# Optimization experiments

Hardware: AMD Instinct MI355X
Metric: run time of the kernel (lower is better)

Reference implementation:

```python
import jax, jax.numpy as jnp
import numpy as np

B_, C_, H_, W_ = 8, 512, 64, 64

def conv1x1(x, W, b):
    # 1x1 conv == per-pixel linear: [B,C,H,W] x [O,C] -> [B,O,H,W]
    return jnp.einsum('bchw,oc->bohw', x, W) + b[None, :, None, None]

def setup_inputs() -> dict:
    key = jax.random.key(0)
    ks = jax.random.split(key, 7)
    s = 1.0 / np.sqrt(C_)
    return {
        'x': jax.random.normal(ks[0], (B_, C_, H_, W_), dtype=jnp.float32),
        'wA': jax.random.normal(ks[1], (C_, C_), dtype=jnp.float32) * s,
        'bA': jax.random.normal(ks[2], (C_,), dtype=jnp.float32) * s,
        'wB': jax.random.normal(ks[3], (C_, C_), dtype=jnp.float32) * s,
        'bB': jax.random.normal(ks[4], (C_,), dtype=jnp.float32) * s,
        'wV': jax.random.normal(ks[5], (C_, C_), dtype=jnp.float32) * s,
        'bV': jax.random.normal(ks[6], (C_,), dtype=jnp.float32) * s,
    }

def reference(x, wA, bA, wB, bB, wV, bV):
    b, c, h, w = x.shape
    hw = h * w
    A = conv1x1(x, wA, bA).reshape(b, c, hw)                      # feature maps
    Bm = jax.nn.softmax(conv1x1(x, wB, bB).reshape(b, c, hw), axis=-1)  # attention maps
    # global_descriptors[b,i,j] = mean_hw softmax(B)[b,i,hw] * A[b,j,hw]
    # == fused softmax + batched matmul, avoiding the O(C*C*HW) broadcast.
    gd = jnp.einsum('bik,bjk->bij', Bm, A) / hw                    # [b, c, c]
    av = jax.nn.softmax(conv1x1(x, wV, bV).reshape(b, c, hw), axis=-1)
    # out[b,j,hw] = sum_i av[b,i,hw] * gd[b,i,j]
    out = jnp.einsum('bih,bij->bjh', av, gd)                       # [b, c, hw]
    return out.reshape(b, c, h, w)
```

## Files before the change

kernel.cpp:

```cpp
#include <hip/hip_runtime.h>
#include <math.h>

#define BB 8
#define CC 512
#define HWN 4096

typedef __bf16 bf16x8 __attribute__((ext_vector_type(8)));
typedef __bf16 bf16x4 __attribute__((ext_vector_type(4)));
typedef float f32x4 __attribute__((ext_vector_type(4)));

#define GLOBAL_AS __attribute__((address_space(1)))
#define LDS_AS __attribute__((address_space(3)))

static __device__ __forceinline__ void async_copy16(const void* g, void* l) {
  __builtin_amdgcn_global_load_lds((const GLOBAL_AS unsigned int*)g,
                                   (LDS_AS unsigned int*)l, 16, 0, 0);
}

template <int BIASMODE, typename OUT_T>
__global__ __launch_bounds__(256) void gemm_mfma_bt(
    const __bf16* __restrict__ Ag, const __bf16* __restrict__ Bg,
    const float* __restrict__ bias, OUT_T* __restrict__ Cg,
    int M, int N, int K, long sA, long sB, long sC, float alpha,
    int ksl, long sSlice) {
  __shared__ __bf16 As[2][128][32];
  __shared__ __bf16 Bs[2][128][32];

  const int tid = threadIdx.x;
  const int n0 = blockIdx.x * 128;
  const int m0 = blockIdx.y * 128;
  const int bz = blockIdx.z;
  const int batch = bz / ksl;
  const int slice = bz - batch * ksl;
  const int kLen = K / ksl;
  const int kBeg = slice * kLen, kEnd = kBeg + kLen;
  Ag += (long)batch * sA;
  Bg += (long)batch * sB;
  Cg += (long)batch * sC + (long)slice * sSlice;

  const int lane = tid & 63;
  const int w = tid >> 6;
  const int wr = w >> 1, wc = w & 1;
  const int l15 = lane & 15, quad = lane >> 4;

  const int srow = w * 32 + (lane >> 2);
  const int scol = (lane & 3) * 8;

  f32x4 acc[4][4] = {};

  for (int k0 = kBeg; k0 < kEnd; k0 += 64) {
    __syncthreads();
#pragma unroll
    for (int h = 0; h < 2; h++) {
#pragma unroll
      for (int j = 0; j < 2; j++) {
        async_copy16(&Ag[(long)(m0 + srow + j * 16) * K + k0 + h * 32 + scol],
                     (char*)&As[h][0][0] + w * 2048 + j * 1024);
        async_copy16(&Bg[(long)(n0 + srow + j * 16) * K + k0 + h * 32 + scol],
                     (char*)&Bs[h][0][0] + w * 2048 + j * 1024);
      }
    }
    __syncthreads();

#pragma unroll
    for (int h = 0; h < 2; h++) {
      bf16x8 af[4], bfr[4];
#pragma unroll
      for (int t = 0; t < 4; t++) {
        af[t]  = *(const bf16x8*)&As[h][wr * 64 + t * 16 + l15][quad * 8];
        bfr[t] = *(const bf16x8*)&Bs[h][wc * 64 + t * 16 + l15][quad * 8];
      }
#pragma unroll
      for (int ti = 0; ti < 4; ti++)
#pragma unroll
        for (int tj = 0; tj < 4; tj++)
          acc[ti][tj] = __builtin_amdgcn_mfma_f32_16x16x32_bf16(
              af[ti], bfr[tj], acc[ti][tj], 0, 0, 0);
    }
  }

#pragma unroll
  for (int ti = 0; ti < 4; ti++) {
#pragma unroll
    for (int tj = 0; tj < 4; tj++) {
#pragma unroll
      for (int r = 0; r < 4; r++) {
        const int m = m0 + wr * 64 + ti * 16 + quad * 4 + r;
        const int n = n0 + wc * 64 + tj * 16 + l15;
        float v = acc[ti][tj][r];
        if (BIASMODE == 1) v += bias[m];
        Cg[(long)m * N + n] = (OUT_T)(v * alpha);
      }
    }
  }
}

__global__ __launch_bounds__(256) void softmax_dual_bf16(
    __bf16* __restrict__ logits, __bf16* __restrict__ bm) {
  const int row = blockIdx.x;
  const int b = row >> 10, c = row & 1023;
  __bf16* src = logits + ((long)b * 1024 + c) * HWN;
  __bf16* dst = (c < 512) ? (bm + ((long)b * 512 + c) * HWN) : src;
  const int tid = threadIdx.x;

  const bf16x8* p = reinterpret_cast<const bf16x8*>(src);
  bf16x8* q = reinterpret_cast<bf16x8*>(dst);

  float v[16];
  float vmax = -3.0e38f;
#pragma unroll
  for (int i = 0; i < 2; i++) {
    bf16x8 t = p[tid + i * 256];
#pragma unroll
    for (int j = 0; j < 8; j++) {
      v[i * 8 + j] = (float)t[j];
      vmax = fmaxf(vmax, v[i * 8 + j]);
    }
  }
#pragma unroll
  for (int off = 32; off > 0; off >>= 1)
    vmax = fmaxf(vmax, __shfl_xor(vmax, off, 64));

  __shared__ float red[4];
  const int wid = tid >> 6;
  if ((tid & 63) == 0) red[wid] = vmax;
  __syncthreads();
  vmax = fmaxf(fmaxf(red[0], red[1]), fmaxf(red[2], red[3]));
  __syncthreads();

  float s = 0.f;
#pragma unroll
  for (int i = 0; i < 16; i++) {
    v[i] = expf(v[i] - vmax);
    s += v[i];
  }
#pragma unroll
  for (int off = 32; off > 0; off >>= 1) s += __shfl_xor(s, off, 64);
  if ((tid & 63) == 0) red[wid] = s;
  __syncthreads();
  s = (red[0] + red[1]) + (red[2] + red[3]);

  const float inv = 1.0f / s;
#pragma unroll
  for (int i = 0; i < 2; i++) {
    bf16x8 o;
#pragma unroll
    for (int j = 0; j < 8; j++) o[j] = (__bf16)(v[i * 8 + j] * inv);
    q[tid + i * 256] = o;
  }
}

__global__ __launch_bounds__(256) void reduce_partials8b(
    const __bf16* __restrict__ P, __bf16* __restrict__ out) {
  const long i = ((long)blockIdx.x * 256 + threadIdx.x) * 8;
  const int b = (int)(i >> 18);
  const long il = i & 262143;
  const __bf16* p = P + (long)b * 2097152 + il;
  float s[8] = {};
#pragma unroll
  for (int sl = 0; sl < 8; sl++) {
    bf16x8 t = *(const bf16x8*)&p[(long)sl * 262144];
#pragma unroll
    for (int j = 0; j < 8; j++) s[j] += (float)t[j];
  }
  bf16x8 o;
#pragma unroll
  for (int j = 0; j < 8; j++) o[j] = (__bf16)s[j];
  *(bf16x8*)&out[i] = o;
}

__global__ __launch_bounds__(256) void convert_all(
    const float* __restrict__ x, __bf16* __restrict__ xb,
    __bf16* __restrict__ xT, const float* __restrict__ wA,
    const float* __restrict__ wB, const float* __restrict__ wV,
    const float* __restrict__ bB, const float* __restrict__ bV,
    __bf16* __restrict__ wAb, __bf16* __restrict__ wBVb,
    float* __restrict__ bBV) {
  if (blockIdx.z == 8) {
    const int t = blockIdx.y * 64 + blockIdx.x;
    const int grp = t >> 7;
    const int r = t & 127;
    if (grp == 3) {
      if (r == 0) {
#pragma unroll
        for (int j = 0; j < 4; j++) {
          const int i = threadIdx.x * 4 + j;
          bBV[i] = (i < 512) ? bB[i] : bV[i - 512];
        }
      }
      return;
    }
    const float* in = grp == 0 ? wB : (grp == 1 ? wV : wA);
    __bf16* o = grp == 0 ? wBVb : (grp == 1 ? wBVb + 262144 : wAb);
    const long base = (long)r * 2048 + threadIdx.x * 8;
    float4 v0 = *(const float4*)&in[base];
    float4 v1 = *(const float4*)&in[base + 4];
    bf16x8 ob;
    ob[0] = (__bf16)v0.x; ob[1] = (__bf16)v0.y; ob[2] = (__bf16)v0.z;
    ob[3] = (__bf16)v0.w; ob[4] = (__bf16)v1.x; ob[5] = (__bf16)v1.y;
    ob[6] = (__bf16)v1.z; ob[7] = (__bf16)v1.w;
    *(bf16x8*)&o[base] = ob;
    return;
  }

  __shared__ __bf16 t[64][66];
  const int j0 = blockIdx.x * 64;
  const int c0 = blockIdx.y * 64;
  const long bofs = (long)blockIdx.z * CC * HWN;
  const int j = threadIdx.x & 63;
  const int g = threadIdx.x >> 6;

#pragma unroll
  for (int r = 0; r < 16; r++) {
    const int i = r * 4 + g;
    const float v = x[bofs + (long)(c0 + i) * HWN + j0 + j];
    const __bf16 bv = (__bf16)v;
    xb[bofs + (long)(c0 + i) * HWN + j0 + j] = bv;
    t[j][i] = bv;
  }
  __syncthreads();
#pragma unroll
  for (int r = 0; r < 16; r++) {
    const int jj = r * 4 + g;
    xT[bofs + (long)(j0 + jj) * CC + c0 + j] = t[jj][j];
  }
}

__global__ __launch_bounds__(256) void transpose_bf16_s(
    const __bf16* __restrict__ in, __bf16* __restrict__ out, int ldIn,
    long sIn, long sOut) {
  __shared__ __bf16 t[64][66];
  const int j0 = blockIdx.x * 64;
  const int c0 = blockIdx.y * 64;
  const int j = threadIdx.x & 63;
  const int g = threadIdx.x >> 6;

#pragma unroll
  for (int r = 0; r < 16; r++) {
    const int i = r * 4 + g;
    t[j][i] = in[(long)blockIdx.z * sIn + (long)(c0 + i) * ldIn + j0 + j];
  }
  __syncthreads();
#pragma unroll
  for (int r = 0; r < 16; r++) {
    const int jj = r * 4 + g;
    out[(long)blockIdx.z * sOut + (long)(j0 + jj) * CC + c0 + j] = t[jj][j];
  }
}

extern "C" void kernel_launch(void* const* d_in, const int* in_sizes, int n_in,
                              void* d_out, int out_size, void* d_ws,
                              size_t ws_size, hipStream_t stream) {
  const float* x  = (const float*)d_in[0];
  const float* wA = (const float*)d_in[1];
  const float* bA = (const float*)d_in[2];
  const float* wB = (const float*)d_in[3];
  const float* bB = (const float*)d_in[4];
  const float* wV = (const float*)d_in[5];
  const float* bV = (const float*)d_in[6];
  float* out = (float*)d_out;

  const size_t nBCHW = (size_t)BB * CC * HWN;
  const size_t nBCC  = (size_t)BB * CC * CC;
  __bf16* xb   = (__bf16*)d_ws;
  __bf16* xT   = xb + nBCHW;
  __bf16* bm   = xT + nBCHW;
  __bf16* Mb   = bm + nBCHW;
  __bf16* gdT  = Mb + nBCC;
  __bf16* wBVb = gdT + nBCC;
  __bf16* wAb  = wBVb + (size_t)1024 * CC;
  float*  bBV  = (float*)(wAb + (size_t)CC * CC);

  const long sBC_HW = (long)CC * HWN;
  const long sCC = (long)CC * CC;

  convert_all<<<dim3(HWN / 64, CC / 64, BB + 1), 256, 0, stream>>>(
      x, xb, xT, wA, wB, wV, bB, bV, wAb, wBVb, bBV);

  __bf16* logits = (__bf16*)d_out;

  gemm_mfma_bt<1, __bf16><<<dim3(HWN / 128, 1024 / 128, BB), 256, 0, stream>>>(
      wBVb, xT, bBV, logits, 1024, HWN, CC, 0, sBC_HW, (long)1024 * HWN, 1.0f,
      1, 0);
  softmax_dual_bf16<<<dim3(BB * 1024), 256, 0, stream>>>(logits, bm);
  transpose_bf16_s<<<dim3(HWN / 64, CC / 64, BB), 256, 0, stream>>>(
      logits + 2097152, xT, HWN, (long)1024 * HWN, (long)HWN * CC);
  gemm_mfma_bt<0, __bf16><<<dim3(CC / 128, CC / 128, BB * 8), 256, 0,
                            stream>>>(bm, xb, nullptr, (__bf16*)out, CC, CC,
                                      HWN, sBC_HW, sBC_HW, (long)2097152,
                                      1.0f, 8, (long)262144);
  reduce_partials8b<<<dim3(1024), 256, 0, stream>>>((const __bf16*)out, Mb);
  gemm_mfma_bt<1, __bf16><<<dim3(CC / 128, CC / 128, BB), 256, 0, stream>>>(
      wAb, Mb, bA, gdT, CC, CC, CC, 0, sCC, sCC, 1.0f / (float)HWN, 1, 0);
  gemm_mfma_bt<0, float><<<dim3(HWN / 128, CC / 128, BB), 256, 0, stream>>>(
      gdT, xT, nullptr, out, CC, HWN, CC, sCC, sBC_HW, sBC_HW, 1.0f, 1, 0);
}
```

Measured before the change: 299.9 us.

## Pipeline GEMM K-loop with 4-stage async LDS buffering and vmcnt waits

Measured after the change: 303.5 us. No clear change (+1.2%).

```diff
diff --git a/kernel.cpp b/kernel.cpp
--- a/kernel.cpp
+++ b/kernel.cpp
@@ -23,8 +23,8 @@
     const float* __restrict__ bias, OUT_T* __restrict__ Cg,
     int M, int N, int K, long sA, long sB, long sC, float alpha,
     int ksl, long sSlice) {
-  __shared__ __bf16 As[2][128][32];
-  __shared__ __bf16 Bs[2][128][32];
+  __shared__ __align__(16) __bf16 As[4][128][32];
+  __shared__ __align__(16) __bf16 Bs[4][128][32];
 
   const int tid = threadIdx.x;
   const int n0 = blockIdx.x * 128;
@@ -33,7 +33,8 @@
   const int batch = bz / ksl;
   const int slice = bz - batch * ksl;
   const int kLen = K / ksl;
-  const int kBeg = slice * kLen, kEnd = kBeg + kLen;
+  const int kBeg = slice * kLen;
+  const int NT = kLen >> 5;
   Ag += (long)batch * sA;
   Bg += (long)batch * sB;
   Cg += (long)batch * sC + (long)slice * sSlice;
@@ -43,40 +44,56 @@
   const int wr = w >> 1, wc = w & 1;
   const int l15 = lane & 15, quad = lane >> 4;
 
-  const int srow = w * 32 + (lane >> 2);
-  const int scol = (lane & 3) * 8;
+  const int srow = tid >> 2;
+  const int scol = (tid & 3) * 8;
+  const __bf16* Arow = Ag + (long)(m0 + srow) * K + scol;
+  const __bf16* Brow = Bg + (long)(n0 + srow) * K + scol;
 
   f32x4 acc[4][4] = {};
 
-  for (int k0 = kBeg; k0 < kEnd; k0 += 64) {
-    __syncthreads();
-#pragma unroll
-    for (int h = 0; h < 2; h++) {
-#pragma unroll
-      for (int j = 0; j < 2; j++) {
-        async_copy16(&Ag[(long)(m0 + srow + j * 16) * K + k0 + h * 32 + scol],
-                     (char*)&As[h][0][0] + w * 2048 + j * 1024);
-        async_copy16(&Bg[(long)(n0 + srow + j * 16) * K + k0 + h * 32 + scol],
-                     (char*)&Bs[h][0][0] + w * 2048 + j * 1024);
-      }
-    }
-    __syncthreads();
-
-#pragma unroll
-    for (int h = 0; h < 2; h++) {
-      bf16x8 af[4], bfr[4];
-#pragma unroll
-      for (int t = 0; t < 4; t++) {
-        af[t]  = *(const bf16x8*)&As[h][wr * 64 + t * 16 + l15][quad * 8];
-        bfr[t] = *(const bf16x8*)&Bs[h][wc * 64 + t * 16 + l15][quad * 8];
-      }
-#pragma unroll
-      for (int ti = 0; ti < 4; ti++)
-#pragma unroll
-        for (int tj = 0; tj < 4; tj++)
-          acc[ti][tj] = __builtin_amdgcn_mfma_f32_16x16x32_bf16(
-              af[ti], bfr[tj], acc[ti][tj], 0, 0, 0);
-    }
+  auto stageT = [&](int t) {
+    const int b = t & 3;
+    const int kk = kBeg + t * 32;
+#pragma unroll
+    for (int s = 0; s < 2; s++) {
+      async_copy16(Arow + (long)s * 64 * K + kk,
+                   (char*)&As[b][0][0] + s * 4096 + tid * 16);
+      async_copy16(Brow + (long)s * 64 * K + kk,
+                   (char*)&Bs[b][0][0] + s * 4096 + tid * 16);
+    }
+  };
+
+  stageT(0);
+  if (NT > 1) stageT(1);
+  if (NT > 2) stageT(2);
+
+  for (int t = 0; t < NT; t++) {
+    if (t < NT - 2)
+      asm volatile("s_waitcnt vmcnt(8)" ::: "memory");
+    else if (t == NT - 2)
+      asm volatile("s_waitcnt vmcnt(4)" ::: "memory");
+    else
+      asm volatile("s_waitcnt vmcnt(0)" ::: "memory");
+    __builtin_amdgcn_s_barrier();
+    __builtin_amdgcn_sched_barrier(0);
+
+    if (t + 3 < NT) stageT(t + 3);
+
+    const int b = t & 3;
+    bf16x8 af[4], bfr[4];
+#pragma unroll
+    for (int u = 0; u < 4; u++) {
+      af[u]  = *(const bf16x8*)&As[b][wr * 64 + u * 16 + l15][quad * 8];
+      bfr[u] = *(const bf16x8*)&Bs[b][wc * 64 + u * 16 + l15][quad * 8];
+    }
+    __builtin_amdgcn_s_setprio(1);
+#pragma unroll
+    for (int ti = 0; ti < 4; ti++)
+#pragma unroll
+      for (int tj = 0; tj < 4; tj++)
+        acc[ti][tj] = __builtin_amdgcn_mfma_f32_16x16x32_bf16(
+            af[ti], bfr[tj], acc[ti][tj], 0, 0, 0);
+    __builtin_amdgcn_s_setprio(0);
   }
 
 #pragma unroll
```
